# Optimization experiments

Hardware: AMD Instinct MI355X
Metric: run time of the kernel (lower is better)

Reference implementation:

```python
import jax, jax.numpy as jnp
import numpy as np

BITS = 8
STEP = 2.0 ** (-5)
QMIN = -2.0 ** (BITS - 1)
QMAX = 2.0 ** (BITS - 1) - 1


def _q(x):
    # DFXP fixed-point fake-quantize: clamp(round(x/step), qmin, qmax)*step
    return jnp.clip(jnp.round(x / STEP), QMIN, QMAX) * STEP


@jax.custom_vjp
def fq(x):
    # ForwardQuantizer: quantize in fwd, straight-through grad
    return _q(x)

def _fq_fwd(x):
    return _q(x), None

def _fq_bwd(_, g):
    return (g,)

fq.defvjp(_fq_fwd, _fq_bwd)


def gq(x):
    # BackwardQuantizer: identity in forward (grad quantized only in bwd pass)
    return x


def setup_inputs() -> dict:
    key = jax.random.key(0)
    ks = jax.random.split(key, 5)
    B, I, H = 2048, 1024, 1024
    return {
        "X": jax.random.normal(ks[0], (B, I), dtype=jnp.float32),
        "h": jax.random.normal(ks[1], (B, H), dtype=jnp.float32),
        "c": jax.random.normal(ks[2], (B, H), dtype=jnp.float32),
        "weight": jax.random.normal(ks[3], (4 * H, I + H), dtype=jnp.float32) * (H ** -0.5),
        "bias": jax.random.normal(ks[4], (4 * H,), dtype=jnp.float32) * (H ** -0.5),
    }


def reference(X, h, c, weight, bias):
    # concat + input/weight/bias fake-quant
    Xh = fq(jnp.concatenate([X, h], axis=1))          # [B, I+H]
    Wq = fq(weight)                                    # [4H, I+H]
    bq = fq(bias)                                      # [4H]
    y = gq(Xh @ Wq.T + bq)                             # [B, 4H]
    i, f, g, o = jnp.split(y, 4, axis=1)
    i = fq(gq(jax.nn.sigmoid(i)))
    f = fq(gq(jax.nn.sigmoid(f)))
    g = fq(gq(jnp.tanh(g)))
    o = fq(gq(jax.nn.sigmoid(o)))
    cq = fq(c)
    c_new = gq(cq * f) + gq(i * g)
    cell_tanh = fq(gq(jnp.tanh(c_new)))
    h_new = gq(cell_tanh * o)
    return (h_new, c_new)
```

## Files before the change

kernel.cpp:

```cpp
#include <hip/hip_runtime.h>
#include <stdint.h>

#define B_DIM 2048
#define K_DIM 2048
#define N_PACK 4096

typedef int v4i __attribute__((ext_vector_type(4)));

__device__ __forceinline__ float fqf(float x) {
    float q = rintf(x * 32.0f);
    q = fminf(fmaxf(q, -128.0f), 127.0f);
    return q * 0.03125f;
}
__device__ __forceinline__ int q8i(float x) {
    float q = rintf(x * 32.0f);
    q = fminf(fmaxf(q, -128.0f), 127.0f);
    return (int)q;
}
__device__ __forceinline__ float fsigm(float x) {
    return __fdividef(1.0f, 1.0f + __expf(-x));
}
__device__ __forceinline__ float ftanh(float x) {
    return __fdividef(2.0f, 1.0f + __expf(-2.0f * x)) - 1.0f;
}

__global__ __launch_bounds__(256) void quant_pack(
    const float* __restrict__ X, const float* __restrict__ hI,
    const float* __restrict__ W, const float* __restrict__ bias,
    int8_t* __restrict__ Xhq, int8_t* __restrict__ Wq, float* __restrict__ bqp)
{
    const int bid = blockIdx.x;
    const int t = threadIdx.x;
    if (bid < B_DIM) {
        const int m = bid;
        const int k0 = t * 8;
        const float* src = (k0 < 1024) ? (X + (size_t)m * 1024 + k0)
                                       : (hI + (size_t)m * 1024 + (k0 - 1024));
        float4 v0 = *(const float4*)src;
        float4 v1 = *(const float4*)(src + 4);
        union { int8_t c[8]; int64_t ll; } u;
        u.c[0] = (int8_t)q8i(v0.x); u.c[1] = (int8_t)q8i(v0.y);
        u.c[2] = (int8_t)q8i(v0.z); u.c[3] = (int8_t)q8i(v0.w);
        u.c[4] = (int8_t)q8i(v1.x); u.c[5] = (int8_t)q8i(v1.y);
        u.c[6] = (int8_t)q8i(v1.z); u.c[7] = (int8_t)q8i(v1.w);
        *(int64_t*)(Xhq + (size_t)m * K_DIM + k0) = u.ll;
    } else if (bid < B_DIM + N_PACK) {
        const int r = bid - B_DIM;
        const int gate = r >> 10, j = r & 1023;
        const int p = (j << 2) | gate;
        const int k0 = t * 8;
        const float* src = W + (size_t)r * K_DIM + k0;
        float4 v0 = *(const float4*)src;
        float4 v1 = *(const float4*)(src + 4);
        union { int8_t c[8]; int64_t ll; } u;
        u.c[0] = (int8_t)q8i(v0.x); u.c[1] = (int8_t)q8i(v0.y);
        u.c[2] = (int8_t)q8i(v0.z); u.c[3] = (int8_t)q8i(v0.w);
        u.c[4] = (int8_t)q8i(v1.x); u.c[5] = (int8_t)q8i(v1.y);
        u.c[6] = (int8_t)q8i(v1.z); u.c[7] = (int8_t)q8i(v1.w);
        *(int64_t*)(Wq + (size_t)p * K_DIM + k0) = u.ll;
    } else {
        for (int idx = t; idx < N_PACK; idx += 256) {
            const int gate = idx >> 10, j = idx & 1023;
            bqp[(j << 2) | gate] = fqf(bias[idx]);
        }
    }
}

__global__ __launch_bounds__(512) void lstm_gemm(
    const int8_t* __restrict__ Xhq, const int8_t* __restrict__ Wq,
    const float* __restrict__ bqp, const float* __restrict__ cin,
    float* __restrict__ hout, float* __restrict__ cout_)
{
    __shared__ __align__(16) char raw[65536];
    const int t = threadIdx.x;
    const int l = t & 63;
    const int wave = t >> 6;
    const int wm = wave >> 2;
    const int wn = wave & 3;

    const int b = blockIdx.x;
    const int xcd = b & 7;
    const int slot = b >> 3;
    const int mt = ((xcd & 1) << 3) + (slot & 7);
    const int nt = ((xcd >> 1) << 3) + (slot >> 3);
    const int m0 = mt * 128;
    const int n0 = nt * 128;

    v4i acc[4][2];
    #pragma unroll
    for (int i = 0; i < 4; ++i)
        #pragma unroll
        for (int j = 0; j < 2; ++j)
            acc[i][j] = (v4i)0;

    const int srow = t >> 3;
    const int schunk = (t & 7) ^ (srow & 7);
    const int8_t* gA = Xhq + (size_t)(m0 + srow) * K_DIM + schunk * 16;
    const int8_t* gB = Wq  + (size_t)(n0 + srow) * K_DIM + schunk * 16;

    const int rrow = l & 15;
    const int lx = l & 7;

#define STAGE(p, kt) do { \
    char* Ad_ = raw + (p) * 32768; \
    char* Bd_ = raw + (p) * 32768 + 16384; \
    _Pragma("unroll") \
    for (int i_ = 0; i_ < 2; ++i_) { \
        __builtin_amdgcn_global_load_lds( \
            (const __attribute__((address_space(1))) uint32_t*)(gA + (size_t)(i_ * 64) * K_DIM + (kt) * 128), \
            (__attribute__((address_space(3))) uint32_t*)(Ad_ + i_ * 8192 + t * 16), 16, 0, 0); \
        __builtin_amdgcn_global_load_lds( \
            (const __attribute__((address_space(1))) uint32_t*)(gB + (size_t)(i_ * 64) * K_DIM + (kt) * 128), \
            (__attribute__((address_space(3))) uint32_t*)(Bd_ + i_ * 8192 + t * 16), 16, 0, 0); \
    } \
} while (0)

    STAGE(0, 0);

    for (int kt = 0; kt < 16; ++kt) {
        const int p = kt & 1;
        if (kt < 15) {
            STAGE(p ^ 1, kt + 1);
            asm volatile("s_waitcnt vmcnt(4)" ::: "memory");
        } else {
            asm volatile("s_waitcnt vmcnt(0)" ::: "memory");
        }
        asm volatile("s_barrier" ::: "memory");

        const char* As = raw + p * 32768;
        const char* Bs = raw + p * 32768 + 16384;
        v4i a[2][4], b2[2][2];
        #pragma unroll
        for (int kk = 0; kk < 2; ++kk) {
            const int c = kk * 4 + (l >> 4);
            const int sl = (c ^ lx) * 16;
            #pragma unroll
            for (int mf = 0; mf < 4; ++mf) {
                const int r = wm * 64 + mf * 16 + rrow;
                a[kk][mf] = *(const v4i*)(As + r * 128 + sl);
            }
            #pragma unroll
            for (int nf = 0; nf < 2; ++nf) {
                const int r = wn * 32 + nf * 16 + rrow;
                b2[kk][nf] = *(const v4i*)(Bs + r * 128 + sl);
            }
        }
        #pragma unroll
        for (int kk = 0; kk < 2; ++kk)
            #pragma unroll
            for (int mf = 0; mf < 4; ++mf)
                #pragma unroll
                for (int nf = 0; nf < 2; ++nf)
                    acc[mf][nf] = __builtin_amdgcn_mfma_i32_16x16x64_i8(a[kk][mf], b2[kk][nf], acc[mf][nf], 0, 0, 0);
        asm volatile("s_waitcnt lgkmcnt(0)" ::: "memory");
        asm volatile("s_barrier" ::: "memory");
    }

    float (*Cs)[132] = (float(*)[132])raw;
    const float sc = 0.0009765625f;
    for (int half = 0; half < 2; ++half) {
        __syncthreads();
        if (wm == half) {
            #pragma unroll
            for (int mf = 0; mf < 4; ++mf) {
                const int rb = mf * 16 + ((l >> 4) << 2);
                #pragma unroll
                for (int nf = 0; nf < 2; ++nf) {
                    const int col = wn * 32 + nf * 16 + (l & 15);
                    #pragma unroll
                    for (int rr = 0; rr < 4; ++rr)
                        Cs[rb + rr][col] = (float)acc[mf][nf][rr] * sc;
                }
            }
        }
        __syncthreads();
        #pragma unroll
        for (int it = 0; it < 4; ++it) {
            const int idx = it * 512 + t;
            const int row = idx >> 5;
            const int jl = idx & 31;
            float4 y = *(const float4*)&Cs[row][jl << 2];
            float4 bb = *(const float4*)&bqp[n0 + (jl << 2)];
            const int m = m0 + half * 64 + row;
            const int j = (n0 >> 2) + jl;
            const float ig = fqf(fsigm(y.x + bb.x));
            const float fg = fqf(fsigm(y.y + bb.y));
            const float gg = fqf(ftanh(y.z + bb.z));
            const float og = fqf(fsigm(y.w + bb.w));
            const float cq = fqf(cin[(size_t)m * 1024 + j]);
            const float cn = cq * fg + ig * gg;
            const float hn = fqf(ftanh(cn)) * og;
            hout[(size_t)m * 1024 + j] = hn;
            cout_[(size_t)m * 1024 + j] = cn;
        }
    }
}

extern "C" void kernel_launch(void* const* d_in, const int* in_sizes, int n_in,
                              void* d_out, int out_size, void* d_ws, size_t ws_size,
                              hipStream_t stream) {
    const float* X    = (const float*)d_in[0];
    const float* h    = (const float*)d_in[1];
    const float* c    = (const float*)d_in[2];
    const float* W    = (const float*)d_in[3];
    const float* bias = (const float*)d_in[4];

    float* out   = (float*)d_out;
    float* h_out = out;
    float* c_out = out + (size_t)B_DIM * 1024;

    char* ws = (char*)d_ws;
    int8_t* Xhq = (int8_t*)ws;
    int8_t* Wq  = (int8_t*)(ws + (size_t)4 * 1024 * 1024);
    float*  bqp = (float*)(ws + (size_t)12 * 1024 * 1024);

    quant_pack<<<B_DIM + N_PACK + 1, 256, 0, stream>>>(X, h, W, bias, Xhq, Wq, bqp);

    lstm_gemm<<<512, 512, 0, stream>>>(Xhq, Wq, bqp, c, h_out, c_out);
}
```

Baseline: 41.08 us.

## Use 256x128 tiles with 1024-thread blocks and triple-buffered LDS pipeline

```diff
diff --git a/kernel.cpp b/kernel.cpp
--- a/kernel.cpp
+++ b/kernel.cpp
@@ -66,12 +66,12 @@
     }
 }
 
-__global__ __launch_bounds__(512) void lstm_gemm(
+__global__ __launch_bounds__(1024, 1) void lstm_gemm(
     const int8_t* __restrict__ Xhq, const int8_t* __restrict__ Wq,
     const float* __restrict__ bqp, const float* __restrict__ cin,
     float* __restrict__ hout, float* __restrict__ cout_)
 {
-    __shared__ __align__(16) char raw[65536];
+    __shared__ __align__(16) char raw[147456];
     const int t = threadIdx.x;
     const int l = t & 63;
     const int wave = t >> 6;
@@ -81,9 +81,9 @@
     const int b = blockIdx.x;
     const int xcd = b & 7;
     const int slot = b >> 3;
-    const int mt = ((xcd & 1) << 3) + (slot & 7);
-    const int nt = ((xcd >> 1) << 3) + (slot >> 3);
-    const int m0 = mt * 128;
+    const int mt = ((xcd & 1) << 2) + (slot & 3);
+    const int nt = ((xcd >> 1) << 3) + (slot >> 2);
+    const int m0 = mt * 256;
     const int n0 = nt * 128;
 
     v4i acc[4][2];
@@ -98,69 +98,66 @@
     const int8_t* gA = Xhq + (size_t)(m0 + srow) * K_DIM + schunk * 16;
     const int8_t* gB = Wq  + (size_t)(n0 + srow) * K_DIM + schunk * 16;
 
+#define STAGE(sb, kt) do { \
+    _Pragma("unroll") \
+    for (int i_ = 0; i_ < 2; ++i_) \
+        __builtin_amdgcn_global_load_lds( \
+            (const __attribute__((address_space(1))) uint32_t*)(gA + (size_t)(i_ * 128) * K_DIM + (size_t)(kt) * 128), \
+            (__attribute__((address_space(3))) uint32_t*)(raw + (sb) + i_ * 16384 + t * 16), 16, 0, 0); \
+    __builtin_amdgcn_global_load_lds( \
+        (const __attribute__((address_space(1))) uint32_t*)(gB + (size_t)(kt) * 128), \
+        (__attribute__((address_space(3))) uint32_t*)(raw + (sb) + 32768 + t * 16), 16, 0, 0); \
+} while (0)
+
+    STAGE(0, 0); STAGE(49152, 1);
+
     const int rrow = l & 15;
     const int lx = l & 7;
-
-#define STAGE(p, kt) do { \
-    char* Ad_ = raw + (p) * 32768; \
-    char* Bd_ = raw + (p) * 32768 + 16384; \
-    _Pragma("unroll") \
-    for (int i_ = 0; i_ < 2; ++i_) { \
-        __builtin_amdgcn_global_load_lds( \
-            (const __attribute__((address_space(1))) uint32_t*)(gA + (size_t)(i_ * 64) * K_DIM + (kt) * 128), \
-            (__attribute__((address_space(3))) uint32_t*)(Ad_ + i_ * 8192 + t * 16), 16, 0, 0); \
-        __builtin_amdgcn_global_load_lds( \
-            (const __attribute__((address_space(1))) uint32_t*)(gB + (size_t)(i_ * 64) * K_DIM + (kt) * 128), \
-            (__attribute__((address_space(3))) uint32_t*)(Bd_ + i_ * 8192 + t * 16), 16, 0, 0); \
-    } \
-} while (0)
-
-    STAGE(0, 0);
-
+    const int g4 = l >> 4;
+
+    int sC = 0;
+    int sN = 98304;
     for (int kt = 0; kt < 16; ++kt) {
-        const int p = kt & 1;
-        if (kt < 15) {
-            STAGE(p ^ 1, kt + 1);
-            asm volatile("s_waitcnt vmcnt(4)" ::: "memory");
-        } else {
-            asm volatile("s_waitcnt vmcnt(0)" ::: "memory");
-        }
+        if (kt < 15) asm volatile("s_waitcnt vmcnt(3)" ::: "memory");
+        else         asm volatile("s_waitcnt vmcnt(0)" ::: "memory");
         asm volatile("s_barrier" ::: "memory");
-
-        const char* As = raw + p * 32768;
-        const char* Bs = raw + p * 32768 + 16384;
+        if (kt < 14) STAGE(sN, kt + 2);
+
+        const char* As = raw + sC;
+        const char* Bs = As + 32768;
         v4i a[2][4], b2[2][2];
         #pragma unroll
         for (int kk = 0; kk < 2; ++kk) {
-            const int c = kk * 4 + (l >> 4);
-            const int sl = (c ^ lx) * 16;
-            #pragma unroll
-            for (int mf = 0; mf < 4; ++mf) {
-                const int r = wm * 64 + mf * 16 + rrow;
-                a[kk][mf] = *(const v4i*)(As + r * 128 + sl);
-            }
-            #pragma unroll
-            for (int nf = 0; nf < 2; ++nf) {
-                const int r = wn * 32 + nf * 16 + rrow;
-                b2[kk][nf] = *(const v4i*)(Bs + r * 128 + sl);
-            }
-        }
+            const int sl = ((kk * 4 + g4) ^ lx) * 16;
+            #pragma unroll
+            for (int mf = 0; mf < 4; ++mf)
+                a[kk][mf] = *(const v4i*)(As + (wm * 64 + mf * 16 + rrow) * 128 + sl);
+            #pragma unroll
+            for (int nf = 0; nf < 2; ++nf)
+                b2[kk][nf] = *(const v4i*)(Bs + (wn * 32 + nf * 16 + rrow) * 128 + sl);
+        }
+        __builtin_amdgcn_s_setprio(1);
         #pragma unroll
         for (int kk = 0; kk < 2; ++kk)
             #pragma unroll
             for (int mf = 0; mf < 4; ++mf)
                 #pragma unroll
                 for (int nf = 0; nf < 2; ++nf)
-                    acc[mf][nf] = __builtin_amdgcn_mfma_i32_16x16x64_i8(a[kk][mf], b2[kk][nf], acc[mf][nf], 0, 0, 0);
-        asm volatile("s_waitcnt lgkmcnt(0)" ::: "memory");
-        asm volatile("s_barrier" ::: "memory");
+                    acc[mf][nf] = __builtin_amdgcn_mfma_i32_16x16x64_i8(
+                        a[kk][mf], b2[kk][nf], acc[mf][nf], 0, 0, 0);
+        __builtin_amdgcn_s_setprio(0);
+
+        sC += 49152; if (sC == 147456) sC = 0;
+        sN += 49152; if (sN == 147456) sN = 0;
     }
+
+#undef STAGE
 
     float (*Cs)[132] = (float(*)[132])raw;
     const float sc = 0.0009765625f;
-    for (int half = 0; half < 2; ++half) {
+    for (int r = 0; r < 4; ++r) {
         __syncthreads();
-        if (wm == half) {
+        if (wm == r) {
             #pragma unroll
             for (int mf = 0; mf < 4; ++mf) {
                 const int rb = mf * 16 + ((l >> 4) << 2);
@@ -175,13 +172,13 @@
         }
         __syncthreads();
         #pragma unroll
-        for (int it = 0; it < 4; ++it) {
-            const int idx = it * 512 + t;
+        for (int it = 0; it < 2; ++it) {
+            const int idx = it * 1024 + t;
             const int row = idx >> 5;
             const int jl = idx & 31;
             float4 y = *(const float4*)&Cs[row][jl << 2];
             float4 bb = *(const float4*)&bqp[n0 + (jl << 2)];
-            const int m = m0 + half * 64 + row;
+            const int m = m0 + r * 64 + row;
             const int j = (n0 >> 2) + jl;
             const float ig = fqf(fsigm(y.x + bb.x));
             const float fg = fqf(fsigm(y.y + bb.y));
@@ -216,5 +213,5 @@
 
     quant_pack<<<B_DIM + N_PACK + 1, 256, 0, stream>>>(X, h, W, bias, Xhq, Wq, bqp);
 
-    lstm_gemm<<<512, 512, 0, stream>>>(Xhq, Wq, bqp, c, h_out, c_out);
-}
+    lstm_gemm<<<256, 1024, 0, stream>>>(Xhq, Wq, bqp, c, h_out, c_out);
+}
```

Measured after the change: 42.13 us. +2.6%, slower.
